# Optimization experiments

Hardware: AMD Instinct MI355X
Metric: run time of the kernel (lower is better)

## Reference

```python
import jax, jax.numpy as jnp
import numpy as np

B, S, H = 2, 2048, 1024
NH = 16
HD = H // NH  # 64


def _linear_params(key, fan_in, fan_out):
    k1, k2 = jax.random.split(key)
    bound = 1.0 / np.sqrt(fan_in)
    W = jax.random.uniform(k1, (fan_in, fan_out), jnp.float32, -bound, bound)
    b = jax.random.uniform(k2, (fan_out,), jnp.float32, -bound, bound)
    return W, b


def setup_inputs() -> dict:
    key = jax.random.key(0)
    ks = jax.random.split(key, 7)
    hidden_states = jax.random.normal(ks[0], (B, S, H), jnp.float32)
    governance_embeddings = jax.random.normal(ks[1], (B, H), jnp.float32)
    Wq, bq = _linear_params(ks[2], H, H)
    Wk, bk = _linear_params(ks[3], H, H)
    Wv, bv = _linear_params(ks[4], H, H)
    Wgq, bgq = _linear_params(ks[5], H, H)
    Wgk, bgk = _linear_params(ks[6], H, H)
    return {
        'hidden_states': hidden_states,
        'governance_embeddings': governance_embeddings,
        'Wq': Wq, 'bq': bq, 'Wk': Wk, 'bk': bk, 'Wv': Wv, 'bv': bv,
        'Wgq': Wgq, 'bgq': bgq, 'Wgk': Wgk, 'bgk': bgk,
    }


def reference(hidden_states, governance_embeddings, Wq, bq, Wk, bk, Wv, bv, Wgq, bgq, Wgk, bgk):
    b, s, h = hidden_states.shape
    # QKV projections -> [b, nh, s, hd]
    def heads(x):
        return x.reshape(b, s, NH, HD).transpose(0, 2, 1, 3)
    q = heads(hidden_states @ Wq + bq)
    k = heads(hidden_states @ Wk + bk)
    v = heads(hidden_states @ Wv + bv)

    scale = jnp.float32(1.0 / np.sqrt(HD))
    scores = jnp.einsum('bhid,bhjd->bhij', q, k) * scale  # [b,nh,s,s]

    # governance bias: one query per example vs per-token keys (unscaled)
    gq = (governance_embeddings @ Wgq + bgq).reshape(b, NH, HD)      # [b,nh,hd]
    gk = (hidden_states @ Wgk + bgk).reshape(b, s, NH, HD)           # [b,s,nh,hd]
    gov_scores = jnp.einsum('bhd,bshd->bhs', gq, gk)                 # [b,nh,s]

    # bias is constant along key dim (torch expand on last axis)
    combined = scores + 0.1 * gov_scores[..., :, None]

    probs = jax.nn.softmax(combined, axis=-1)  # dropout = identity (eval)
    context = jnp.einsum('bhij,bhjd->bhid', probs, v)
    context = context.transpose(0, 2, 1, 3).reshape(b, s, h)

    entropy = -jnp.sum(probs * jnp.log(probs + 1e-8), axis=-1).mean()
    influence = jnp.abs(gov_scores).mean()  # mean over expanded tensor == mean over [b,nh,s]
    concentration = probs.max(axis=-1).mean()
    return context, entropy, influence, concentration
```

## Files before the change

### kernel.cpp

```cpp
#include <hip/hip_runtime.h>


typedef unsigned short u16;
typedef __attribute__((ext_vector_type(8))) short bf16x8;
typedef __attribute__((ext_vector_type(4))) float f32x4;
typedef __attribute__((ext_vector_type(16))) float f32x16;
typedef __attribute__((ext_vector_type(2))) float f32x2;
typedef __attribute__((ext_vector_type(4))) u16 u16x4;
typedef __attribute__((ext_vector_type(4))) float float4v;

typedef const __attribute__((address_space(1))) void gvoid_t;
typedef __attribute__((address_space(3))) void lvoid_t;

__device__ __forceinline__ void gl_lds16(const void* g, void* l) {
  __builtin_amdgcn_global_load_lds((gvoid_t*)g, (lvoid_t*)l, 16, 0, 0);
}

__device__ __forceinline__ u16 f2bf(float x) {
  union { float f; unsigned u; } v; v.f = x;
  unsigned r = v.u + 0x7fffu + ((v.u >> 16) & 1u);
  return (u16)(r >> 16);
}
__device__ __forceinline__ float bf2f(u16 h) {
  union { unsigned u; float f; } v; v.u = ((unsigned)h) << 16; return v.f;
}
__device__ __forceinline__ unsigned pk2(float hi, float lo) {
  union { float f; unsigned u; } a, b; a.f = hi; b.f = lo;
  return __builtin_amdgcn_perm(a.u, b.u, 0x07060302u);
}
__device__ __forceinline__ bf16x8 mk8(unsigned a, unsigned b, unsigned c, unsigned d) {
  union { unsigned u[4]; bf16x8 v; } x;
  x.u[0] = a; x.u[1] = b; x.u[2] = c; x.u[3] = d; return x.v;
}

#if defined(__has_builtin)
#if __has_builtin(__builtin_amdgcn_exp2f)
#define EXP2(x) __builtin_amdgcn_exp2f(x)
#endif
#endif
#ifndef EXP2
#define EXP2(x) exp2f(x)
#endif

__global__ void prep(const float* __restrict__ hs,
                     const float* __restrict__ W0, const float* __restrict__ W1,
                     const float* __restrict__ W2, const float* __restrict__ W3,
                     const float* __restrict__ ge, const float* __restrict__ Wgq,
                     u16* __restrict__ hsB, u16* __restrict__ WB,
                     float* __restrict__ gq_part, float* __restrict__ acc3) {
  __shared__ __align__(16) u16 T[64][72];
  int bx = blockIdx.x, tid = threadIdx.x;
  if (bx < 2048) {
    int i = bx * 256 + tid;
    const float4v* in4 = (const float4v*)hs;
    float4v a = in4[i * 2], b = in4[i * 2 + 1];
    bf16x8 v;
    v[0] = (short)f2bf(a.x); v[1] = (short)f2bf(a.y);
    v[2] = (short)f2bf(a.z); v[3] = (short)f2bf(a.w);
    v[4] = (short)f2bf(b.x); v[5] = (short)f2bf(b.y);
    v[6] = (short)f2bf(b.z); v[7] = (short)f2bf(b.w);
    *(bf16x8*)&hsB[(size_t)i * 8] = v;
    return;
  }
  if (bx < 3072) {
    int idx = bx - 2048;
    int mat = idx >> 8, sub = idx & 255;
    const float* W = (mat == 0) ? W0 : (mat == 1) ? W1 : (mat == 2) ? W2 : W3;
    int k0 = (sub >> 4) * 64, n0 = (sub & 15) * 64;
#pragma unroll
    for (int p = 0; p < 4; ++p) {
      int chunk = p * 256 + tid;
      int row = chunk >> 4, cp = chunk & 15;
      float4v v = *(const float4v*)&W[(size_t)(k0 + row) * 1024 + n0 + cp * 4];
      u16x4 o; o.x = f2bf(v.x); o.y = f2bf(v.y); o.z = f2bf(v.z); o.w = f2bf(v.w);
      *(u16x4*)&T[row][cp * 4] = o;
    }
    __syncthreads();
#pragma unroll
    for (int p = 0; p < 2; ++p) {
      int chunk = p * 256 + tid;
      int nrow = chunk >> 3, cp = chunk & 7;
      bf16x8 v;
#pragma unroll
      for (int e = 0; e < 8; ++e) v[e] = (short)T[cp * 8 + e][nrow];
      *(bf16x8*)&WB[(size_t)(mat * 1024 + n0 + nrow) * 1024 + k0 + cp * 8] = v;
    }
    return;
  }
  {
    int idx = bx - 3072;
    if (idx == 0 && tid < 3) acc3[tid] = 0.f;
    int kb = idx >> 1, b = idx & 1;
    int col0 = tid * 4;
    float4v s = {0.f, 0.f, 0.f, 0.f};
    for (int k = kb * 32; k < kb * 32 + 32; ++k) {
      float g = ge[b * 1024 + k];
      float4v w = *(const float4v*)&Wgq[(size_t)k * 1024 + col0];
      s.x += g * w.x; s.y += g * w.y; s.z += g * w.z; s.w += g * w.w;
    }
    *(float4v*)&gq_part[(size_t)idx * 1024 + col0] = s;
  }
}

__global__ __launch_bounds__(256, 3) void gemm_qkvg(
    const u16* __restrict__ A, const u16* __restrict__ Bw,
    const float* __restrict__ bq, const float* __restrict__ bk,
    const float* __restrict__ bv, const float* __restrict__ bgk,
    const float* __restrict__ bgq, const float* __restrict__ gq_part,
    u16* __restrict__ Qb, u16* __restrict__ Kb, u16* __restrict__ Vt,
    float* __restrict__ acc3) {
  __shared__ __align__(16) u16 As[2][128 * 32];
  __shared__ __align__(16) u16 Bs[2][128 * 32];
  __shared__ float redI[4];
  const int tid = threadIdx.x, lane = tid & 63, wv = tid >> 6;
  const int li = lane & 15, quad = lane >> 4;
  const int bid = blockIdx.x;
  const int nb = bid & 31, mb = bid >> 5;
  const u16* Ap = A + (size_t)(mb * 128) * 1024;
  const u16* Bp = Bw + (size_t)(nb * 128) * 1024;
  const int wm0 = (wv >> 1) * 64, wn0 = (wv & 1) * 64;

  f32x4 acc[4][4];
#pragma unroll
  for (int t = 0; t < 4; ++t)
#pragma unroll
    for (int u = 0; u < 4; ++u) acc[t][u] = (f32x4){0.f, 0.f, 0.f, 0.f};

#pragma unroll
  for (int jj = 0; jj < 2; ++jj) {
    int j = wv * 2 + jj;
    int row = j * 16 + (lane >> 2);
    int co = lane & 3;
    gl_lds16(Ap + (size_t)row * 1024 + co * 8, &As[0][j * 512]);
    gl_lds16(Bp + (size_t)row * 1024 + co * 8, &Bs[0][j * 512]);
  }

  for (int kt = 0; kt < 32; ++kt) {
    const int cur = kt & 1;
    __syncthreads();
    if (kt < 31) {
#pragma unroll
      for (int jj = 0; jj < 2; ++jj) {
        int j = wv * 2 + jj;
        int row = j * 16 + (lane >> 2);
        int co = lane & 3;
        gl_lds16(Ap + (size_t)row * 1024 + (kt + 1) * 32 + co * 8, &As[cur ^ 1][j * 512]);
        gl_lds16(Bp + (size_t)row * 1024 + (kt + 1) * 32 + co * 8, &Bs[cur ^ 1][j * 512]);
      }
    }
    bf16x8 af[4], bf[4];
#pragma unroll
    for (int t = 0; t < 4; ++t)
      af[t] = *(const bf16x8*)&As[cur][(wm0 + t * 16 + li) * 32 + quad * 8];
#pragma unroll
    for (int u = 0; u < 4; ++u)
      bf[u] = *(const bf16x8*)&Bs[cur][(wn0 + u * 16 + li) * 32 + quad * 8];
#pragma unroll
    for (int t = 0; t < 4; ++t)
#pragma unroll
      for (int u = 0; u < 4; ++u)
        acc[t][u] = __builtin_amdgcn_mfma_f32_16x16x32_bf16(af[t], bf[u], acc[t][u], 0, 0, 0);
  }

  const int nbase = nb * 128;
  const int mat = nbase >> 10;
  if (mat == 3) {
    const int colbase = nbase & 1023;
    const int bat = (mb * 128) >> 11;
    float gqv[4], bgkv[4];
#pragma unroll
    for (int u2 = 0; u2 < 4; ++u2) {
      int col = colbase + wn0 + u2 * 16 + li;
      float g = bgq[col];
      for (int kb = 0; kb < 32; ++kb)
        g += gq_part[(size_t)(kb * 2 + bat) * 1024 + col];
      gqv[u2] = g;
      bgkv[u2] = bgk[col];
    }
    float infl = 0.f;
#pragma unroll
    for (int t = 0; t < 4; ++t)
#pragma unroll
      for (int r = 0; r < 4; ++r) {
        float v = (acc[t][0][r] + bgkv[0]) * gqv[0];
        v = __builtin_fmaf(acc[t][1][r] + bgkv[1], gqv[1], v);
        v = __builtin_fmaf(acc[t][2][r] + bgkv[2], gqv[2], v);
        v = __builtin_fmaf(acc[t][3][r] + bgkv[3], gqv[3], v);
        v += __shfl_xor(v, 1, 64); v += __shfl_xor(v, 2, 64);
        v += __shfl_xor(v, 4, 64); v += __shfl_xor(v, 8, 64);
        infl += fabsf(v);
      }
    infl = (li == 0) ? infl : 0.f;
    infl += __shfl_xor(infl, 16, 64);
    infl += __shfl_xor(infl, 32, 64);
    if (lane == 0) redI[wv] = infl;
    __syncthreads();
    if (tid == 0) atomicAdd(&acc3[2], redI[0] + redI[1] + redI[2] + redI[3]);
  } else if (mat == 2) {
#pragma unroll
    for (int t = 0; t < 4; ++t)
#pragma unroll
      for (int u = 0; u < 4; ++u) {
        int col = (nbase & 1023) + wn0 + u * 16 + li;
        float bb = bv[col];
        int row = mb * 128 + wm0 + t * 16 + quad * 4;
        int b = row >> 11, s = row & 2047;
        uint2 w;
        w.x = pk2(acc[t][u][1] + bb, acc[t][u][0] + bb);
        w.y = pk2(acc[t][u][3] + bb, acc[t][u][2] + bb);
        *(uint2*)&Vt[(size_t)b * (1024 * 2048) + (size_t)col * 2048 + s] = w;
      }
  } else {
    const float* bias = (mat == 0) ? bq : bk;
    u16* outp = (mat == 0) ? Qb : Kb;
    const float qscale = (mat == 0) ? 0.18033688f : 1.0f;
#pragma unroll
    for (int t = 0; t < 4; ++t)
#pragma unroll
      for (int u = 0; u < 4; ++u) {
        int col = (nbase & 1023) + wn0 + u * 16 + li;
        float bb = bias[col];
#pragma unroll
        for (int r = 0; r < 4; ++r) {
          int row = mb * 128 + wm0 + t * 16 + quad * 4 + r;
          outp[(size_t)row * 1024 + col] = f2bf((acc[t][u][r] + bb) * qscale);
        }
      }
  }
}

__global__ __launch_bounds__(256, 2) void attn_kernel(
    const u16* __restrict__ Qb, const u16* __restrict__ Kb,
    const u16* __restrict__ Vt, float* __restrict__ out,
    float* __restrict__ acc3 ) {
  __shared__ __align__(16) u16 Ks[2][128 * 64];
  __shared__ __align__(16) u16 Vs[2][64 * 128];
  __shared__ float red[8];

  const int tid = threadIdx.x, lane = tid & 63, wv = tid >> 6;
  const int q_l = lane & 31, half = lane >> 5;
  const int bx = blockIdx.x;
  const int bh = bx & 31, qb = bx >> 5;
  const int b = bh >> 4, h = bh & 15;

  const u16* Qp = Qb + (size_t)(b * 2048 + qb * 128 + wv * 32 + q_l) * 1024 + h * 64;
  const u16* Kp = Kb + (size_t)(b * 2048) * 1024 + h * 64;
  const u16* Vp = Vt + (size_t)b * (1024 * 2048) + (size_t)(h * 64) * 2048;

  bf16x8 qf[4];
#pragma unroll
  for (int s = 0; s < 4; ++s)
    qf[s] = *(const bf16x8*)&Qp[s * 16 + half * 8];

  f32x2 mx2 = {-3.0e38f, -3.0e38f}, ps2 = {0.f, 0.f}, es2 = {0.f, 0.f};
  f32x16 accO[2];
#pragma unroll
  for (int dt = 0; dt < 2; ++dt)
#pragma unroll
    for (int r = 0; r < 16; ++r) accO[dt][r] = 0.f;

#pragma unroll
  for (int jj = 0; jj < 4; ++jj) {
    int j = wv * 4 + jj;
    int row = j * 8 + (lane >> 3);
    int c16 = (lane & 7) ^ (row & 7);
    gl_lds16(Kp + (size_t)row * 1024 + c16 * 8, &Ks[0][j * 512]);
  }
#pragma unroll
  for (int jj = 0; jj < 4; ++jj) {
    int j = wv * 4 + jj;
    int row = j * 4 + (lane >> 4);
    int c16 = (lane & 15) ^ (row & 7);
    gl_lds16(Vp + (size_t)row * 2048 + c16 * 8, &Vs[0][j * 512]);
  }

  for (int kt = 0; kt < 16; ++kt) {
    const int cur = kt & 1;
    __syncthreads();
    if (kt < 15) {
      const u16* Kpt = Kp + (size_t)((kt + 1) * 128) * 1024;
#pragma unroll
      for (int jj = 0; jj < 4; ++jj) {
        int j = wv * 4 + jj;
        int row = j * 8 + (lane >> 3);
        int c16 = (lane & 7) ^ (row & 7);
        gl_lds16(Kpt + (size_t)row * 1024 + c16 * 8, &Ks[cur ^ 1][j * 512]);
      }
#pragma unroll
      for (int jj = 0; jj < 4; ++jj) {
        int j = wv * 4 + jj;
        int row = j * 4 + (lane >> 4);
        int c16 = (lane & 15) ^ (row & 7);
        gl_lds16(Vp + (size_t)row * 2048 + (kt + 1) * 128 + c16 * 8, &Vs[cur ^ 1][j * 512]);
      }
    }
    const u16* KsC = &Ks[cur][0];
    const u16* VsC = &Vs[cur][0];

#pragma unroll
    for (int u = 0; u < 4; ++u) {
      f32x16 c;
#pragma unroll
      for (int r = 0; r < 16; ++r) c[r] = 0.f;
#pragma unroll
      for (int s = 0; s < 4; ++s) {
        int p = (2 * s + half) ^ (q_l & 7);
        bf16x8 a = *(const bf16x8*)&KsC[(u * 32 + q_l) * 64 + p * 8];
        c = __builtin_amdgcn_mfma_f32_32x32x16_bf16(a, qf[s], c, 0, 0, 0);
      }
#pragma unroll
      for (int r = 0; r < 8; ++r) {
        f32x2 sv = {c[2 * r], c[2 * r + 1]};
        mx2 = __builtin_elementwise_max(mx2, sv);
        f32x2 pe = {EXP2(sv.x), EXP2(sv.y)};
        ps2 += pe;
        es2 += pe * sv;
        c[2 * r] = pe.x; c[2 * r + 1] = pe.y;
      }
      bf16x8 bf0 = mk8(pk2(c[1], c[0]),   pk2(c[3], c[2]),
                       pk2(c[5], c[4]),   pk2(c[7], c[6]));
      bf16x8 bf1 = mk8(pk2(c[9], c[8]),   pk2(c[11], c[10]),
                       pk2(c[13], c[12]), pk2(c[15], c[14]));
#pragma unroll
      for (int dt = 0; dt < 2; ++dt) {
        int d = dt * 32 + q_l, dx = d & 7;
        const u16* vr = &VsC[d * 128 + half * 4];
        uint2 a0 = *(const uint2*)&vr[((u * 4 + 0) ^ dx) * 8];
        uint2 a1 = *(const uint2*)&vr[((u * 4 + 1) ^ dx) * 8];
        accO[dt] = __builtin_amdgcn_mfma_f32_32x32x16_bf16(
            mk8(a0.x, a0.y, a1.x, a1.y), bf0, accO[dt], 0, 0, 0);
        uint2 a2 = *(const uint2*)&vr[((u * 4 + 2) ^ dx) * 8];
        uint2 a3 = *(const uint2*)&vr[((u * 4 + 3) ^ dx) * 8];
        accO[dt] = __builtin_amdgcn_mfma_f32_32x32x16_bf16(
            mk8(a2.x, a2.y, a3.x, a3.y), bf1, accO[dt], 0, 0, 0);
      }
    }
  }

  float l_st = ps2.x + ps2.y, e_st = es2.x + es2.y, m_st = fmaxf(mx2.x, mx2.y);
  float lsum = l_st + __shfl_xor(l_st, 32, 64);
  float esum = e_st + __shfl_xor(e_st, 32, 64);
  float mm = fmaxf(m_st, __shfl_xor(m_st, 32, 64));
  float inv = 1.0f / lsum;
  float entw = __logf(lsum) - 0.69314718f * esum * inv;
  float concw = EXP2(mm) * inv;

  float* outp = out + (size_t)(b * 2048 + qb * 128 + wv * 32 + q_l) * 1024 + h * 64;
#pragma unroll
  for (int dt = 0; dt < 2; ++dt)
#pragma unroll
    for (int g = 0; g < 4; ++g) {
      float4v o;
      o.x = accO[dt][4 * g + 0] * inv; o.y = accO[dt][4 * g + 1] * inv;
      o.z = accO[dt][4 * g + 2] * inv; o.w = accO[dt][4 * g + 3] * inv;
      *(float4v*)&outp[dt * 32 + 8 * g + 4 * half] = o;
    }

#pragma unroll
  for (int off = 1; off < 64; off <<= 1) {
    entw += __shfl_xor(entw, off, 64);
    concw += __shfl_xor(concw, off, 64);
  }
  if (lane == 0) { red[wv] = entw * 0.5f; red[4 + wv] = concw * 0.5f; }
  __syncthreads();
  if (tid == 0) {
    atomicAdd(&acc3[0], red[0] + red[1] + red[2] + red[3]);
    atomicAdd(&acc3[1], red[4] + red[5] + red[6] + red[7]);
  }
}

__global__ void finalize(const float* __restrict__ acc3, float* __restrict__ out) {
  if (threadIdx.x == 0) {
    out[0] = acc3[0] * (1.f / 65536.f);
    out[1] = acc3[2] * (1.f / 65536.f);
    out[2] = acc3[1] * (1.f / 65536.f);
  }
}

extern "C" void kernel_launch(void* const* d_in, const int* in_sizes, int n_in,
                              void* d_out, int out_size, void* d_ws, size_t ws_size,
                              hipStream_t stream) {
  (void)in_sizes; (void)n_in; (void)out_size; (void)ws_size;
  const float* hs  = (const float*)d_in[0];
  const float* ge  = (const float*)d_in[1];
  const float* Wq  = (const float*)d_in[2];
  const float* bq  = (const float*)d_in[3];
  const float* Wk  = (const float*)d_in[4];
  const float* bk  = (const float*)d_in[5];
  const float* Wv  = (const float*)d_in[6];
  const float* bv  = (const float*)d_in[7];
  const float* Wgq = (const float*)d_in[8];
  const float* bgq = (const float*)d_in[9];
  const float* Wgk = (const float*)d_in[10];
  const float* bgk = (const float*)d_in[11];

  char* ws = (char*)d_ws;
  u16* hsB = (u16*)(ws);
  u16* WB  = (u16*)(ws + (size_t)(8 << 20));
  u16* Qb  = (u16*)(ws + (size_t)(16 << 20));
  u16* Kb  = (u16*)(ws + (size_t)(24 << 20));
  u16* Vt  = (u16*)(ws + (size_t)(32 << 20));
  float* gq_part = (float*)(ws + (size_t)(48 << 20));
  float* acc3    = (float*)(ws + (size_t)(48 << 20) + 524288);
  float* out = (float*)d_out;

  prep<<<3136, 256, 0, stream>>>(hs, Wq, Wk, Wv, Wgk, ge, Wgq, hsB, WB, gq_part, acc3);
  gemm_qkvg<<<1024, 256, 0, stream>>>(hsB, WB, bq, bk, bv, bgk, bgq, gq_part,
                                      Qb, Kb, Vt, acc3);
  attn_kernel<<<512, 256, 0, stream>>>(Qb, Kb, Vt, out, acc3);
  finalize<<<1, 64, 0, stream>>>(acc3, out + 4194304);
}
```

Baseline: 209.5 us.

## Store K and V in 4-element-grouped interleaved layouts for attention tiles

After: 208.0 us. About the same (-0.7%).

```diff
diff --git a/kernel.cpp b/kernel.cpp
--- a/kernel.cpp
+++ b/kernel.cpp
@@ -20,9 +20,6 @@
   union { float f; unsigned u; } v; v.f = x;
   unsigned r = v.u + 0x7fffu + ((v.u >> 16) & 1u);
   return (u16)(r >> 16);
-}
-__device__ __forceinline__ float bf2f(u16 h) {
-  union { unsigned u; float f; } v; v.u = ((unsigned)h) << 16; return v.f;
 }
 __device__ __forceinline__ unsigned pk2(float hi, float lo) {
   union { float f; unsigned u; } a, b; a.f = hi; b.f = lo;
@@ -107,7 +104,7 @@
     const float* __restrict__ bq, const float* __restrict__ bk,
     const float* __restrict__ bv, const float* __restrict__ bgk,
     const float* __restrict__ bgq, const float* __restrict__ gq_part,
-    u16* __restrict__ Qb, u16* __restrict__ Kb, u16* __restrict__ Vt,
+    u16* __restrict__ Qb, u16* __restrict__ Kt4, u16* __restrict__ Vt4,
     float* __restrict__ acc3) {
   __shared__ __align__(16) u16 As[2][128 * 32];
   __shared__ __align__(16) u16 Bs[2][128 * 32];
@@ -204,48 +201,62 @@
         int col = (nbase & 1023) + wn0 + u * 16 + li;
         float bb = bv[col];
         int row = mb * 128 + wm0 + t * 16 + quad * 4;
-        int b = row >> 11, s = row & 2047;
+        int b = row >> 11, s = row & 2047, g = s >> 2;
         uint2 w;
         w.x = pk2(acc[t][u][1] + bb, acc[t][u][0] + bb);
         w.y = pk2(acc[t][u][3] + bb, acc[t][u][2] + bb);
-        *(uint2*)&Vt[(size_t)b * (1024 * 2048) + (size_t)col * 2048 + s] = w;
-      }
-  } else {
-    const float* bias = (mat == 0) ? bq : bk;
-    u16* outp = (mat == 0) ? Qb : Kb;
-    const float qscale = (mat == 0) ? 0.18033688f : 1.0f;
+        *(uint2*)&Vt4[(((size_t)b * 512 + g) * 1024 + col) * 4] = w;
+      }
+  } else if (mat == 1) {
 #pragma unroll
     for (int t = 0; t < 4; ++t)
 #pragma unroll
       for (int u = 0; u < 4; ++u) {
         int col = (nbase & 1023) + wn0 + u * 16 + li;
-        float bb = bias[col];
+        int h = col >> 6, g = (col & 63) >> 2, r4 = col & 3;
+        float bb = bk[col];
+        u16* base = &Kt4[(((size_t)(0 * 16 + h) * 16 + g) * 2048) * 4 + r4];
 #pragma unroll
         for (int r = 0; r < 4; ++r) {
           int row = mb * 128 + wm0 + t * 16 + quad * 4 + r;
-          outp[(size_t)row * 1024 + col] = f2bf((acc[t][u][r] + bb) * qscale);
+          int b = row >> 11, s = row & 2047;
+          base[((size_t)b * 16 * 16 * 2048 + s) * 4] = f2bf(acc[t][u][r] + bb);
         }
       }
+  } else {
+#pragma unroll
+    for (int t = 0; t < 4; ++t)
+#pragma unroll
+      for (int u = 0; u < 4; ++u) {
+        int col = (nbase & 1023) + wn0 + u * 16 + li;
+        float bb = bq[col];
+#pragma unroll
+        for (int r = 0; r < 4; ++r) {
+          int row = mb * 128 + wm0 + t * 16 + quad * 4 + r;
+          Qb[(size_t)row * 1024 + col] = f2bf((acc[t][u][r] + bb) * 0.18033688f);
+        }
+      }
   }
 }
 
 __global__ __launch_bounds__(256, 2) void attn_kernel(
-    const u16* __restrict__ Qb, const u16* __restrict__ Kb,
-    const u16* __restrict__ Vt, float* __restrict__ out,
+    const u16* __restrict__ Qb, const u16* __restrict__ Kt4,
+    const u16* __restrict__ Vt4, float* __restrict__ out,
     float* __restrict__ acc3 ) {
-  __shared__ __align__(16) u16 Ks[2][128 * 64];
-  __shared__ __align__(16) u16 Vs[2][64 * 128];
+  __shared__ __align__(16) u16 Ks[2][8192];
+  __shared__ __align__(16) u16 Vs[2][8192];
   __shared__ float red[8];
 
   const int tid = threadIdx.x, lane = tid & 63, wv = tid >> 6;
   const int q_l = lane & 31, half = lane >> 5;
+  const int x8 = half << 3;
   const int bx = blockIdx.x;
   const int bh = bx & 31, qb = bx >> 5;
   const int b = bh >> 4, h = bh & 15;
 
   const u16* Qp = Qb + (size_t)(b * 2048 + qb * 128 + wv * 32 + q_l) * 1024 + h * 64;
-  const u16* Kp = Kb + (size_t)(b * 2048) * 1024 + h * 64;
-  const u16* Vp = Vt + (size_t)b * (1024 * 2048) + (size_t)(h * 64) * 2048;
+  const u16* Kp4 = Kt4 + ((size_t)(b * 16 + h) * 16) * 2048 * 4;
+  const u16* Vp4 = Vt4 + ((size_t)b * 512 * 1024 + h * 64) * 4;
 
   bf16x8 qf[4];
 #pragma unroll
@@ -259,39 +270,41 @@
 #pragma unroll
     for (int r = 0; r < 16; ++r) accO[dt][r] = 0.f;
 
+  const int ksrc = (2 * lane);
+  const int vlane_d = 2 * (lane & 31);
+
+#pragma unroll
+  for (int jj = 0; jj < 4; ++jj) {
+    int g = wv * 4 + jj;
+    int xg = ((g >> 1) & 1) << 3;
+    gl_lds16(Kp4 + ((size_t)g * 2048 + (ksrc ^ xg)) * 4, &Ks[0][g * 512]);
+  }
 #pragma unroll
   for (int jj = 0; jj < 4; ++jj) {
     int j = wv * 4 + jj;
-    int row = j * 8 + (lane >> 3);
-    int c16 = (lane & 7) ^ (row & 7);
-    gl_lds16(Kp + (size_t)row * 1024 + c16 * 8, &Ks[0][j * 512]);
-  }
-#pragma unroll
-  for (int jj = 0; jj < 4; ++jj) {
-    int j = wv * 4 + jj;
-    int row = j * 4 + (lane >> 4);
-    int c16 = (lane & 15) ^ (row & 7);
-    gl_lds16(Vp + (size_t)row * 2048 + c16 * 8, &Vs[0][j * 512]);
+    int g = 2 * j + (lane >> 5);
+    int xg = (g & 1) << 3;
+    gl_lds16(Vp4 + ((size_t)g * 1024 + (vlane_d ^ xg)) * 4, &Vs[0][j * 512]);
   }
 
   for (int kt = 0; kt < 16; ++kt) {
     const int cur = kt & 1;
     __syncthreads();
     if (kt < 15) {
-      const u16* Kpt = Kp + (size_t)((kt + 1) * 128) * 1024;
+#pragma unroll
+      for (int jj = 0; jj < 4; ++jj) {
+        int g = wv * 4 + jj;
+        int xg = ((g >> 1) & 1) << 3;
+        gl_lds16(Kp4 + ((size_t)g * 2048 + (kt + 1) * 128 + (ksrc ^ xg)) * 4,
+                 &Ks[cur ^ 1][g * 512]);
+      }
 #pragma unroll
       for (int jj = 0; jj < 4; ++jj) {
         int j = wv * 4 + jj;
-        int row = j * 8 + (lane >> 3);
-        int c16 = (lane & 7) ^ (row & 7);
-        gl_lds16(Kpt + (size_t)row * 1024 + c16 * 8, &Ks[cur ^ 1][j * 512]);
-      }
-#pragma unroll
-      for (int jj = 0; jj < 4; ++jj) {
-        int j = wv * 4 + jj;
-        int row = j * 4 + (lane >> 4);
-        int c16 = (lane & 15) ^ (row & 7);
-        gl_lds16(Vp + (size_t)row * 2048 + (kt + 1) * 128 + c16 * 8, &Vs[cur ^ 1][j * 512]);
+        int g = 2 * j + (lane >> 5);
+        int xg = (g & 1) << 3;
+        gl_lds16(Vp4 + ((size_t)((kt + 1) * 32 + g) * 1024 + (vlane_d ^ xg)) * 4,
+                 &Vs[cur ^ 1][j * 512]);
       }
     }
     const u16* KsC = &Ks[cur][0];
@@ -299,14 +312,17 @@
 
 #pragma unroll
     for (int u = 0; u < 4; ++u) {
+      const int keyp = (u * 32 + q_l) ^ x8;
       f32x16 c;
 #pragma unroll
       for (int r = 0; r < 16; ++r) c[r] = 0.f;
 #pragma unroll
       for (int s = 0; s < 4; ++s) {
-        int p = (2 * s + half) ^ (q_l & 7);
-        bf16x8 a = *(const bf16x8*)&KsC[(u * 32 + q_l) * 64 + p * 8];
-        c = __builtin_amdgcn_mfma_f32_32x32x16_bf16(a, qf[s], c, 0, 0, 0);
+        int g0 = s * 4 + half * 2;
+        uint2 k0 = *(const uint2*)&KsC[g0 * 512 + keyp * 4];
+        uint2 k1 = *(const uint2*)&KsC[(g0 + 1) * 512 + keyp * 4];
+        c = __builtin_amdgcn_mfma_f32_32x32x16_bf16(
+            mk8(k0.x, k0.y, k1.x, k1.y), qf[s], c, 0, 0, 0);
       }
 #pragma unroll
       for (int r = 0; r < 8; ++r) {
@@ -323,16 +339,15 @@
                        pk2(c[13], c[12]), pk2(c[15], c[14]));
 #pragma unroll
       for (int dt = 0; dt < 2; ++dt) {
-        int d = dt * 32 + q_l, dx = d & 7;
-        const u16* vr = &VsC[d * 128 + half * 4];
-        uint2 a0 = *(const uint2*)&vr[((u * 4 + 0) ^ dx) * 8];
-        uint2 a1 = *(const uint2*)&vr[((u * 4 + 1) ^ dx) * 8];
+        int dp = (dt * 32 + q_l) ^ x8;
+        uint2 v0 = *(const uint2*)&VsC[(u * 8 + half) * 256 + dp * 4];
+        uint2 v1 = *(const uint2*)&VsC[(u * 8 + 2 + half) * 256 + dp * 4];
         accO[dt] = __builtin_amdgcn_mfma_f32_32x32x16_bf16(
-            mk8(a0.x, a0.y, a1.x, a1.y), bf0, accO[dt], 0, 0, 0);
-        uint2 a2 = *(const uint2*)&vr[((u * 4 + 2) ^ dx) * 8];
-        uint2 a3 = *(const uint2*)&vr[((u * 4 + 3) ^ dx) * 8];
+            mk8(v0.x, v0.y, v1.x, v1.y), bf0, accO[dt], 0, 0, 0);
+        uint2 v2 = *(const uint2*)&VsC[(u * 8 + 4 + half) * 256 + dp * 4];
+        uint2 v3 = *(const uint2*)&VsC[(u * 8 + 6 + half) * 256 + dp * 4];
         accO[dt] = __builtin_amdgcn_mfma_f32_32x32x16_bf16(
-            mk8(a2.x, a2.y, a3.x, a3.y), bf1, accO[dt], 0, 0, 0);
+            mk8(v2.x, v2.y, v3.x, v3.y), bf1, accO[dt], 0, 0, 0);
       }
     }
   }
@@ -395,18 +410,18 @@
   const float* bgk = (const float*)d_in[11];
 
   char* ws = (char*)d_ws;
-  u16* hsB = (u16*)(ws);
-  u16* WB  = (u16*)(ws + (size_t)(8 << 20));
-  u16* Qb  = (u16*)(ws + (size_t)(16 << 20));
-  u16* Kb  = (u16*)(ws + (size_t)(24 << 20));
-  u16* Vt  = (u16*)(ws + (size_t)(32 << 20));
+  u16* hsB  = (u16*)(ws);
+  u16* WB   = (u16*)(ws + (size_t)(8 << 20));
+  u16* Qb   = (u16*)(ws + (size_t)(16 << 20));
+  u16* Kt4  = (u16*)(ws + (size_t)(24 << 20));
+  u16* Vt4  = (u16*)(ws + (size_t)(32 << 20));
   float* gq_part = (float*)(ws + (size_t)(48 << 20));
   float* acc3    = (float*)(ws + (size_t)(48 << 20) + 524288);
   float* out = (float*)d_out;
 
   prep<<<3136, 256, 0, stream>>>(hs, Wq, Wk, Wv, Wgk, ge, Wgq, hsB, WB, gq_part, acc3);
   gemm_qkvg<<<1024, 256, 0, stream>>>(hsB, WB, bq, bk, bv, bgk, bgq, gq_part,
-                                      Qb, Kb, Vt, acc3);
-  attn_kernel<<<512, 256, 0, stream>>>(Qb, Kb, Vt, out, acc3);
+                                      Qb, Kt4, Vt4, acc3);
+  attn_kernel<<<512, 256, 0, stream>>>(Qb, Kt4, Vt4, out, acc3);
   finalize<<<1, 64, 0, stream>>>(acc3, out + 4194304);
 }
```
